# Performance work log

Hardware: AMD Instinct MI355X
Metric: run time of the kernel (lower is better)

The kernel has to match this reference:

```python
import jax, jax.numpy as jnp
import numpy as np

NX, NY = 256, 256            # img_size
NUM_DET, VIEW = 368, 180
SDD, SCD = 1000.0, 500.0
DCD = SDD - SCD
DET_INT = 2.0
PX = 1.0                     # pixel_size
SHIFT = 0.0                  # no quarter offset


def _geometry():
    # Faithful numpy port of FP.param_setting (equally_spaced mode)
    d_beta = np.pi * 360.0 / VIEW / 180.0
    beta = np.linspace(0.0, (VIEW - 1) * d_beta, VIEW)
    axis_x = np.linspace(-NX / 2, NX / 2, NX + 1) * PX          # [NX+1]
    axis_y = np.linspace(-NY / 2, NY / 2, NY + 1) * PX          # [NY+1]
    range_det_x = np.ones(NUM_DET) * DCD
    range_det_y = np.linspace(-(NUM_DET - 1) / 2, (NUM_DET - 1) / 2, NUM_DET) * DET_INT + SHIFT
    src = np.array([-SCD, 0.0])
    cb, sb = np.cos(beta), np.sin(beta)
    src_point = np.stack([src[0] * cb + src[1] * sb, -src[0] * sb + src[1] * cb])  # [2, V]
    det_x_rot = cb[None, :] * range_det_x[:, None] + sb[None, :] * range_det_y[:, None]   # [D, V]
    det_y_rot = -sb[None, :] * range_det_x[:, None] + cb[None, :] * range_det_y[:, None]  # [D, V]
    ax = (axis_x[:, None] - src_point[0][None, :])[None, :, :] / (det_x_rot - src_point[0])[:, None, :]  # [D, NX+1, V]
    ay = (axis_y[:, None] - src_point[1][None, :])[None, :, :] / (det_y_rot - src_point[1])[:, None, :]  # [D, NY+1, V]
    a_min = np.maximum(np.minimum(ax[:, 0, :], ax[:, -1, :]), np.minimum(ay[:, 0, :], ay[:, -1, :]))
    a_min[a_min < 0] = 0.0
    a_max = np.minimum(np.maximum(ax[:, 0, :], ax[:, -1, :]), np.maximum(ay[:, 0, :], ay[:, -1, :]))
    a_max[a_max > 1] = 1.0
    axy = np.concatenate([ax, ay], axis=1)                       # [D, NX+NY+2, V]
    axy[(axy > a_max[:, None, :]) | (axy < a_min[:, None, :])] = np.nan
    axy = np.sort(axy, axis=1)                                   # NaNs sort to the end (matches torch)
    diff_axy = np.diff(axy, n=1, axis=1)                         # [D, S, V], S = NX+NY+1
    a_mid = axy[:, :-1, :] + diff_axy / 2
    diff_axy = np.nan_to_num(diff_axy, nan=0.0)
    a_mid = np.nan_to_num(a_mid, nan=0.0)
    s2d = np.sqrt((det_x_rot - src_point[0]) ** 2 + (det_y_rot - src_point[1]) ** 2)  # [D, V]
    weighting = diff_axy.transpose(0, 2, 1)[None, None] * s2d[None, None, :, :, None]  # [1,1,D,V,S]
    x_pos = a_mid * (det_x_rot[:, None, :] - src_point[0]) + src_point[0]
    x_pos = x_pos.transpose(0, 2, 1) / (PX * (NX - 1) / 2)       # [D, V, S]
    y_pos = a_mid * (det_y_rot[:, None, :] - src_point[1]) + src_point[1]
    y_pos = y_pos.transpose(0, 2, 1) / (PX * (NY - 1) / 2)
    grid_pos = np.stack([x_pos, y_pos], axis=-1)                 # [D, V, S, 2]
    return grid_pos.astype(np.float32), weighting.astype(np.float32)


def _bilinear_sample(img, gx, gy):
    # torch.nn.functional.grid_sample: bilinear, padding_mode='zeros', align_corners=False
    # img: [B,C,H,W]; gx indexes W, gy indexes H; gx/gy: [D,V,S]
    B, C, H, W = img.shape
    ix = ((gx + 1.0) * W - 1.0) * 0.5
    iy = ((gy + 1.0) * H - 1.0) * 0.5
    ix0 = jnp.floor(ix)
    iy0 = jnp.floor(iy)
    wx1 = ix - ix0
    wy1 = iy - iy0
    out = jnp.zeros((B, C) + gx.shape, dtype=img.dtype)
    for dx in (0, 1):
        for dy in (0, 1):
            xi = ix0 + dx
            yi = iy0 + dy
            w = (wx1 if dx else 1.0 - wx1) * (wy1 if dy else 1.0 - wy1)
            valid = (xi >= 0) & (xi < W) & (yi >= 0) & (yi < H)
            xi_c = jnp.clip(xi, 0, W - 1).astype(jnp.int32)
            yi_c = jnp.clip(yi, 0, H - 1).astype(jnp.int32)
            out = out + img[:, :, yi_c, xi_c] * (w * valid)[None, None]
    return out  # [B,C,D,V,S]


def setup_inputs() -> dict:
    key = jax.random.key(0)
    img = jax.random.normal(key, (1, 1, NX, NY), dtype=jnp.float32)
    gp, wt = _geometry()
    return {"img": img, "grid_pos": jnp.asarray(gp), "weighting": jnp.asarray(wt)}


def reference(img, grid_pos, weighting):
    # All views vectorized at once (torch version loops over views)
    interp = _bilinear_sample(img, grid_pos[..., 0], grid_pos[..., 1])  # [B,C,D,V,S]
    sino = jnp.sum(weighting * interp, axis=-1)                         # [B,C,D,V]
    return jnp.where(jnp.isnan(sino), jnp.zeros((), sino.dtype), sino)
```

## Files before the change

kernel.cpp:

```cpp
#include <hip/hip_runtime.h>
#include <hip/hip_fp16.h>
#include <math.h>


constexpr int IMG_N  = 256;
constexpr int NDET   = 368;
constexpr int NVIEW  = 180;
constexpr int NSAMP  = 2 * IMG_N + 1;
constexpr int DV     = NDET * NVIEW;
constexpr int NITER  = (NSAMP + 63) / 64;

struct __align__(8) Corner { __half2 ab; __half2 cd; };

constexpr size_t PACK_BYTES = (size_t)IMG_N * IMG_N * sizeof(Corner);
constexpr size_t RT_OFF     = PACK_BYTES;
constexpr size_t RT_BYTES   = (size_t)DV * 3 * sizeof(float4);
constexpr size_t KR_OFF     = RT_OFF + RT_BYTES;
constexpr size_t KR_BYTES   = (size_t)DV * sizeof(int2);
constexpr size_t WS_NEEDED  = KR_OFF + KR_BYTES;

__device__ __forceinline__ double valAP(double A, double s, double inv, int k) {
    return (A + s * (double)k) * inv;
}

__global__ __launch_bounds__(256) void pack_kernel(
    const float* __restrict__ img, Corner* __restrict__ P)
{
    const int idx = blockIdx.x * 256 + threadIdx.x;
    const int y  = idx >> 8;
    const int x  = idx & 255;
    const int x1 = min(x + 1, IMG_N - 1);
    const int y1 = min(y + 1, IMG_N - 1);
    Corner c;
    c.ab = __floats2half2_rn(img[y * IMG_N + x],  img[y * IMG_N + x1]);
    c.cd = __floats2half2_rn(img[y1 * IMG_N + x], img[y1 * IMG_N + x1]);
    P[idx] = c;
}

__global__ __launch_bounds__(256) void geom_kernel(
    float4* __restrict__ rt, int2* __restrict__ kr)
{
    const int idx = blockIdx.x * 256 + threadIdx.x;
    if (idx >= DV) return;
    const int d = idx / NVIEW;
    const int v = idx - d * NVIEW;

    const double d_beta = ((M_PI * 360.0) / (double)NVIEW) / 180.0;
    const double stop   = (double)(NVIEW - 1) * d_beta;
    const double step   = stop / (double)(NVIEW - 1);
    const double beta   = (v == NVIEW - 1) ? stop : (double)v * step;
    const double cb = cos(beta), sb = sin(beta);

    const double sx  = -500.0 * cb;
    const double sy  =  500.0 * sb;
    const double rdy = ((double)d - 183.5) * 2.0;
    const double dx  = cb * 500.0 + sb * rdy;
    const double dy  = (-sb) * 500.0 + cb * rdy;
    const double ddx = dx - sx, ddy = dy - sy;

    double Ax, sxn;
    const double invx = 1.0 / ddx;
    if (invx >= 0.0) { Ax = -128.0 - sx; sxn = 1.0; }
    else             { Ax =  128.0 - sx; sxn = -1.0; }
    double Ay, syn;
    const double invy = 1.0 / ddy;
    if (invy >= 0.0) { Ay = -128.0 - sy; syn = 1.0; }
    else             { Ay =  128.0 - sy; syn = -1.0; }

    const double vx0 = valAP(Ax, sxn, invx, 0), vxN = valAP(Ax, sxn, invx, IMG_N);
    const double vy0 = valAP(Ay, syn, invy, 0), vyN = valAP(Ay, syn, invy, IMG_N);
    double a_min = fmax(vx0, vy0); if (a_min < 0.0) a_min = 0.0;
    double a_max = fmin(vxN, vyN); if (a_max > 1.0) a_max = 1.0;

    const double absdx = fabs(ddx), absdy = fabs(ddy);

    int klox, khix, kloy, khiy;
    {
        double kd = (a_min - vx0) * absdx;
        kd = fmin(fmax(kd, -1.0), 258.0);
        int k = (int)kd; k = max(0, min(k, 256));
        while (k > 0    && valAP(Ax, sxn, invx, k - 1) >= a_min) --k;
        while (k <= 256 && valAP(Ax, sxn, invx, k) < a_min)      ++k;
        klox = k;
        kd = (a_max - vx0) * absdx;
        kd = fmin(fmax(kd, -1.0), 258.0);
        k = (int)kd; k = max(0, min(k, 256));
        while (k > 0    && valAP(Ax, sxn, invx, k - 1) > a_max)  --k;
        while (k <= 256 && valAP(Ax, sxn, invx, k) <= a_max)     ++k;
        khix = k - 1;
        if (klox > khix) { klox = 0; khix = -1; }
    }
    {
        double kd = (a_min - vy0) * absdy;
        kd = fmin(fmax(kd, -1.0), 258.0);
        int k = (int)kd; k = max(0, min(k, 256));
        while (k > 0    && valAP(Ay, syn, invy, k - 1) >= a_min) --k;
        while (k <= 256 && valAP(Ay, syn, invy, k) < a_min)      ++k;
        kloy = k;
        kd = (a_max - vy0) * absdy;
        kd = fmin(fmax(kd, -1.0), 258.0);
        k = (int)kd; k = max(0, min(k, 256));
        while (k > 0    && valAP(Ay, syn, invy, k - 1) > a_max)  --k;
        while (k <= 256 && valAP(Ay, syn, invy, k) <= a_max)     ++k;
        khiy = k - 1;
        if (kloy > khiy) { kloy = 0; khiy = -1; }
    }

    const int nx = khix - klox + 1;
    const int ny = khiy - kloy + 1;
    const double s2d = sqrt(ddx * ddx + ddy * ddy);

    const double sxd = sxn * invx, syd = syn * invy;
    const double bxd = (Ax + sxn * (double)klox) * invx;
    const double byd = (Ay + syn * (double)kloy) * invy;
    const double ssum = sxd + syd;
    const double c0 = (byd - bxd) / ssum;
    const double c1 = syd / ssum;

    float4* o = rt + (size_t)idx * 3;
    o[0] = make_float4((float)bxd, (float)sxd, (float)byd, (float)syd);
    o[1] = make_float4((float)c0, (float)c1, (float)s2d, 0.0f);
    o[2] = make_float4((float)(ddx * (128.0 / 127.5)),
                       (float)(sx  * (128.0 / 127.5) + 127.5),
                       (float)(ddy * (128.0 / 127.5)),
                       (float)(sy  * (128.0 / 127.5) + 127.5));
    kr[idx] = make_int2(nx, ny);
}

__device__ __forceinline__ float mergedq(int q, float bx, float sx, float by,
                                         float sy, float c0, float c1,
                                         int nx, int ny)
{
    const int t   = q + 1;
    const int mlo = max(0, t - ny);
    const int mhi = min(nx, t);
    int m = (int)fmaf((float)q, c1, c0);
    m = max(mlo, min(m, mhi));
    while (m > mlo) {
        const int mm = m - 1;
        const bool Pmm = (t - 1 - mm < 0) || (mm >= nx) ||
            (fmaf((float)(t - 1 - mm), sy, by) <= fmaf((float)mm, sx, bx));
        if (!Pmm) break;
        m = mm;
    }
    while (m < mhi) {
        const bool Pm = (t - 1 - m < 0) || (m >= nx) ||
            (fmaf((float)(t - 1 - m), sy, by) <= fmaf((float)m, sx, bx));
        if (Pm) break;
        ++m;
    }
    const float xl = (m > 0)     ? fmaf((float)(m - 1),     sx, bx) : -3e38f;
    const float yl = (t - m > 0) ? fmaf((float)(t - 1 - m), sy, by) : -3e38f;
    return fmaxf(xl, yl);
}

__global__ __launch_bounds__(256) void fp_siddon(
    const Corner* __restrict__ P,
    const float4* __restrict__ rt,
    const int2*   __restrict__ kr,
    float*        __restrict__ out)
{
    const int wave = threadIdx.x >> 6;
    const int lane = threadIdx.x & 63;
    const int dv   = __builtin_amdgcn_readfirstlane(blockIdx.x * 4 + wave);

    const float4 A = rt[(size_t)dv * 3 + 0];
    const float4 B = rt[(size_t)dv * 3 + 1];
    const float4 C = rt[(size_t)dv * 3 + 2];
    const int2 nn = kr[dv];
    const int nx = nn.x, ny = nn.y;
    const int M = nx + ny;
    const int npairs = M - 1;

    float acc = 0.0f;

    for (int base = 0; base < npairs; base += 64) {
        const int p = base + lane;
        const bool act = (p < npairs);
        const int q = act ? p + 1 : 1;

        const float cur = mergedq(q, A.x, A.y, A.z, A.w, B.x, B.y, nx, ny);
        float prev = __shfl_up(cur, 1, 64);
        if (lane == 0)
            prev = mergedq(base, A.x, A.y, A.z, A.w, B.x, B.y, nx, ny);

        const float diff = cur - prev;
        const float mid  = fmaf(diff, 0.5f, prev);
        const float ixp  = fmaf(mid, C.x, C.y);
        const float iyp  = fmaf(mid, C.z, C.w);
        const float wf   = act ? diff * B.z : 0.0f;

        const float fx0 = floorf(ixp), fy0 = floorf(iyp);
        const float wx1 = ixp - fx0,  wy1 = iyp - fy0;
        const int x0 = (int)fx0, y0 = (int)fy0;
        const int xc = min(max(x0, 0), IMG_N - 1);
        const int yb = min(max(y0, 0), IMG_N - 1);

        const Corner pc = P[yb * IMG_N + xc];
        const float2 r0 = __half22float2(pc.ab);
        const float2 r1 = __half22float2(pc.cd);

        const bool loX = (x0 == -1), loY = (y0 == -1);
        const float a  = r0.x;
        const float b2 = loX ? r0.x : r0.y;
        const float d2 = loX ? r1.x : r1.y;
        const float c3 = loY ? a  : r1.x;
        const float d3 = loY ? b2 : d2;
        const float x0v = (((unsigned)x0)       < 256u) ? 1.0f : 0.0f;
        const float x1v = (((unsigned)(x0 + 1)) < 256u) ? 1.0f : 0.0f;
        const float my0 = (((unsigned)y0)       < 256u) ? 1.0f : 0.0f;
        const float my1 = (((unsigned)(y0 + 1)) < 256u) ? 1.0f : 0.0f;
        const float wx0 = 1.0f - wx1;
        const float wy0 = (1.0f - wy1) * my0;
        const float wy1m = wy1 * my1;
        const float interp = (a * x0v * wx0 + b2 * x1v * wx1) * wy0
                           + (c3 * x0v * wx0 + d3 * x1v * wx1) * wy1m;

        acc = fmaf(wf, interp, acc);
    }

    #pragma unroll
    for (int off = 32; off > 0; off >>= 1)
        acc += __shfl_down(acc, off, 64);
    if (lane == 0)
        out[dv] = isnan(acc) ? 0.0f : acc;
}

__global__ __launch_bounds__(256) void fp_kernel_nopack(
    const float*  __restrict__ img,
    const float2* __restrict__ grid,
    const float*  __restrict__ wt,
    float*        __restrict__ out)
{
    const int wave = threadIdx.x >> 6;
    const int lane = threadIdx.x & 63;
    const int dv   = blockIdx.x * 4 + wave;
    const long base = (long)dv * NSAMP;

    float2 g[NITER];
    float  w[NITER];
    #pragma unroll
    for (int k = 0; k < NITER; ++k) {
        const int s = lane + k * 64;
        if (s < NSAMP) { g[k] = grid[base + s]; w[k] = wt[base + s]; }
        else           { g[k] = make_float2(0.0f, 0.0f); w[k] = 0.0f; }
    }
    float acc = 0.0f;
    #pragma unroll
    for (int k = 0; k < NITER; ++k) {
        const float ix = ((g[k].x + 1.0f) * 256.0f - 1.0f) * 0.5f;
        const float iy = ((g[k].y + 1.0f) * 256.0f - 1.0f) * 0.5f;
        const float fx0 = floorf(ix), fy0 = floorf(iy);
        const float wx1 = ix - fx0,  wy1 = iy - fy0;
        const int x0 = (int)fx0, y0 = (int)fy0;
        const int xc  = min(max(x0, 0), IMG_N - 2);
        const int yc0 = min(max(y0, 0), IMG_N - 1);
        const int yc1 = min(max(y0 + 1, 0), IMG_N - 1);
        const float2 p0 = *(const float2*)(img + yc0 * IMG_N + xc);
        const float2 p1 = *(const float2*)(img + yc1 * IMG_N + xc);
        const bool x0v = ((unsigned)x0) < 256u;
        const bool x1v = ((unsigned)(x0 + 1)) < 256u;
        const bool hiX = (x0 == IMG_N - 1);
        const bool loX = (x0 == -1);
        const float v00 = x0v ? (hiX ? p0.y : p0.x) : 0.0f;
        const float v01 = x1v ? (loX ? p0.x : p0.y) : 0.0f;
        const float v10 = x0v ? (hiX ? p1.y : p1.x) : 0.0f;
        const float v11 = x1v ? (loX ? p1.x : p1.y) : 0.0f;
        const float my0 = (((unsigned)y0) < 256u) ? 1.0f : 0.0f;
        const float my1 = (((unsigned)(y0 + 1)) < 256u) ? 1.0f : 0.0f;
        const float wx0 = 1.0f - wx1;
        const float wy0 = (1.0f - wy1) * my0;
        const float wy1m = wy1 * my1;
        acc += w[k] * ((v00 * wx0 + v01 * wx1) * wy0
                     + (v10 * wx0 + v11 * wx1) * wy1m);
    }
    #pragma unroll
    for (int off = 32; off > 0; off >>= 1)
        acc += __shfl_down(acc, off, 64);
    if (lane == 0) out[dv] = isnan(acc) ? 0.0f : acc;
}

extern "C" void kernel_launch(void* const* d_in, const int* in_sizes, int n_in,
                              void* d_out, int out_size, void* d_ws, size_t ws_size,
                              hipStream_t stream) {
    const float*  img  = (const float*)d_in[0];
    const float2* grid = (const float2*)d_in[1];
    const float*  wt   = (const float*)d_in[2];
    float*        out  = (float*)d_out;

    if (ws_size >= WS_NEEDED) {
        Corner* P  = (Corner*)d_ws;
        float4* rt = (float4*)((char*)d_ws + RT_OFF);
        int2*   kr = (int2*)  ((char*)d_ws + KR_OFF);
        pack_kernel<<<IMG_N * IMG_N / 256, 256, 0, stream>>>(img, P);
        geom_kernel<<<(DV + 255) / 256, 256, 0, stream>>>(rt, kr);
        fp_siddon<<<DV / 4, 256, 0, stream>>>(P, rt, kr, out);
    } else {
        fp_kernel_nopack<<<DV / 4, 256, 0, stream>>>(img, grid, wt, out);
    }
}
```

Before: 412.7 us.

## Enumerate Siddon crossings per plane with local rank search and transposed corner table

Each lane now owns one crossing (an x-plane or a y-plane index) rather than one position in the merged sorted order. It finds the next crossing with a short local search against the other axis. This removes the merge-rank search over both sequences and the cross-lane shuffle plus the extra lane-0 recompute. A transposed packed corner table is added so lanes on y-plane crossings read a layout whose consecutive samples sit next to each other in memory. This doubles the packing work and the workspace, adds a divergent branch between the x and y paths, and changes tie handling between coincident crossings.

```diff
diff --git a/kernel.cpp b/kernel.cpp
--- a/kernel.cpp
+++ b/kernel.cpp
@@ -13,7 +13,8 @@
 struct __align__(8) Corner { __half2 ab; __half2 cd; };
 
 constexpr size_t PACK_BYTES = (size_t)IMG_N * IMG_N * sizeof(Corner);
-constexpr size_t RT_OFF     = PACK_BYTES;
+constexpr size_t PT_OFF     = PACK_BYTES;
+constexpr size_t RT_OFF     = 2 * PACK_BYTES;
 constexpr size_t RT_BYTES   = (size_t)DV * 3 * sizeof(float4);
 constexpr size_t KR_OFF     = RT_OFF + RT_BYTES;
 constexpr size_t KR_BYTES   = (size_t)DV * sizeof(int2);
@@ -24,17 +25,29 @@
 }
 
 __global__ __launch_bounds__(256) void pack_kernel(
-    const float* __restrict__ img, Corner* __restrict__ P)
+    const float* __restrict__ img, Corner* __restrict__ P, Corner* __restrict__ PT)
 {
     const int idx = blockIdx.x * 256 + threadIdx.x;
-    const int y  = idx >> 8;
-    const int x  = idx & 255;
-    const int x1 = min(x + 1, IMG_N - 1);
-    const int y1 = min(y + 1, IMG_N - 1);
-    Corner c;
-    c.ab = __floats2half2_rn(img[y * IMG_N + x],  img[y * IMG_N + x1]);
-    c.cd = __floats2half2_rn(img[y1 * IMG_N + x], img[y1 * IMG_N + x1]);
-    P[idx] = c;
+    if (idx < IMG_N * IMG_N) {
+        const int y  = idx >> 8;
+        const int x  = idx & 255;
+        const int x1 = min(x + 1, IMG_N - 1);
+        const int y1 = min(y + 1, IMG_N - 1);
+        Corner c;
+        c.ab = __floats2half2_rn(img[y * IMG_N + x],  img[y * IMG_N + x1]);
+        c.cd = __floats2half2_rn(img[y1 * IMG_N + x], img[y1 * IMG_N + x1]);
+        P[idx] = c;
+    } else {
+        const int k  = idx - IMG_N * IMG_N;
+        const int x  = k >> 8;
+        const int y  = k & 255;
+        const int x1 = min(x + 1, IMG_N - 1);
+        const int y1 = min(y + 1, IMG_N - 1);
+        Corner c;
+        c.ab = __floats2half2_rn(img[y * IMG_N + x],  img[y1 * IMG_N + x]);
+        c.cd = __floats2half2_rn(img[y * IMG_N + x1], img[y1 * IMG_N + x1]);
+        PT[k] = c;
+    }
 }
 
 __global__ __launch_bounds__(256) void geom_kernel(
@@ -113,13 +126,12 @@
     const double sxd = sxn * invx, syd = syn * invy;
     const double bxd = (Ax + sxn * (double)klox) * invx;
     const double byd = (Ay + syn * (double)kloy) * invy;
-    const double ssum = sxd + syd;
-    const double c0 = (byd - bxd) / ssum;
-    const double c1 = syd / ssum;
+    const double invsxd = 1.0 / sxd;
+    const double invsyd = 1.0 / syd;
 
     float4* o = rt + (size_t)idx * 3;
     o[0] = make_float4((float)bxd, (float)sxd, (float)byd, (float)syd);
-    o[1] = make_float4((float)c0, (float)c1, (float)s2d, 0.0f);
+    o[1] = make_float4((float)invsxd, (float)invsyd, (float)s2d, 0.0f);
     o[2] = make_float4((float)(ddx * (128.0 / 127.5)),
                        (float)(sx  * (128.0 / 127.5) + 127.5),
                        (float)(ddy * (128.0 / 127.5)),
@@ -127,35 +139,9 @@
     kr[idx] = make_int2(nx, ny);
 }
 
-__device__ __forceinline__ float mergedq(int q, float bx, float sx, float by,
-                                         float sy, float c0, float c1,
-                                         int nx, int ny)
-{
-    const int t   = q + 1;
-    const int mlo = max(0, t - ny);
-    const int mhi = min(nx, t);
-    int m = (int)fmaf((float)q, c1, c0);
-    m = max(mlo, min(m, mhi));
-    while (m > mlo) {
-        const int mm = m - 1;
-        const bool Pmm = (t - 1 - mm < 0) || (mm >= nx) ||
-            (fmaf((float)(t - 1 - mm), sy, by) <= fmaf((float)mm, sx, bx));
-        if (!Pmm) break;
-        m = mm;
-    }
-    while (m < mhi) {
-        const bool Pm = (t - 1 - m < 0) || (m >= nx) ||
-            (fmaf((float)(t - 1 - m), sy, by) <= fmaf((float)m, sx, bx));
-        if (Pm) break;
-        ++m;
-    }
-    const float xl = (m > 0)     ? fmaf((float)(m - 1),     sx, bx) : -3e38f;
-    const float yl = (t - m > 0) ? fmaf((float)(t - 1 - m), sy, by) : -3e38f;
-    return fmaxf(xl, yl);
-}
-
 __global__ __launch_bounds__(256) void fp_siddon(
     const Corner* __restrict__ P,
+    const Corner* __restrict__ PT,
     const float4* __restrict__ rt,
     const int2*   __restrict__ kr,
     float*        __restrict__ out)
@@ -170,35 +156,56 @@
     const int2 nn = kr[dv];
     const int nx = nn.x, ny = nn.y;
     const int M = nx + ny;
-    const int npairs = M - 1;
 
     float acc = 0.0f;
 
-    for (int base = 0; base < npairs; base += 64) {
-        const int p = base + lane;
-        const bool act = (p < npairs);
-        const int q = act ? p + 1 : 1;
-
-        const float cur = mergedq(q, A.x, A.y, A.z, A.w, B.x, B.y, nx, ny);
-        float prev = __shfl_up(cur, 1, 64);
-        if (lane == 0)
-            prev = mergedq(base, A.x, A.y, A.z, A.w, B.x, B.y, nx, ny);
-
-        const float diff = cur - prev;
-        const float mid  = fmaf(diff, 0.5f, prev);
+    for (int base = 0; base < M; base += 64) {
+        int c = base + lane;
+        const bool act = (c < M);
+        c = act ? c : (M - 1);
+        const bool isX = (c < nx);
+
+        float cur, nxt;
+        if (isX) {
+            cur = fmaf((float)c, A.y, A.x);
+            int j = (int)((cur - A.z) * B.y);
+            j = max(0, min(j, ny));
+            while (j > 0  && fmaf((float)(j - 1), A.w, A.z) >= cur) --j;
+            while (j < ny && fmaf((float)j,       A.w, A.z) <  cur) ++j;
+            nxt = 3.0e38f;
+            if (c + 1 < nx) nxt = fmaf((float)(c + 1), A.y, A.x);
+            if (j < ny)     nxt = fminf(nxt, fmaf((float)j, A.w, A.z));
+        } else {
+            const int cy = c - nx;
+            cur = fmaf((float)cy, A.w, A.z);
+            int i = (int)((cur - A.x) * B.x);
+            i = max(0, min(i, nx));
+            while (i > 0  && fmaf((float)(i - 1), A.y, A.x) >  cur) --i;
+            while (i < nx && fmaf((float)i,       A.y, A.x) <= cur) ++i;
+            nxt = 3.0e38f;
+            if (cy + 1 < ny) nxt = fmaf((float)(cy + 1), A.w, A.z);
+            if (i < nx)      nxt = fminf(nxt, fmaf((float)i, A.y, A.x));
+        }
+
+        const bool valid = act && (nxt < 2.9e38f);
+        if (!valid) nxt = cur;
+        const float diff = nxt - cur;
+        const float mid  = fmaf(diff, 0.5f, cur);
+        const float wf   = valid ? diff * B.z : 0.0f;
         const float ixp  = fmaf(mid, C.x, C.y);
         const float iyp  = fmaf(mid, C.z, C.w);
-        const float wf   = act ? diff * B.z : 0.0f;
 
         const float fx0 = floorf(ixp), fy0 = floorf(iyp);
         const float wx1 = ixp - fx0,  wy1 = iyp - fy0;
         const int x0 = (int)fx0, y0 = (int)fy0;
         const int xc = min(max(x0, 0), IMG_N - 1);
-        const int yb = min(max(y0, 0), IMG_N - 1);
-
-        const Corner pc = P[yb * IMG_N + xc];
-        const float2 r0 = __half22float2(pc.ab);
-        const float2 r1 = __half22float2(pc.cd);
+        const int yc = min(max(y0, 0), IMG_N - 1);
+
+        const Corner pc = isX ? P[(yc << 8) + xc] : PT[(xc << 8) + yc];
+        const float2 u  = __half22float2(pc.ab);
+        const float2 w2 = __half22float2(pc.cd);
+        const float2 r0 = isX ? u  : make_float2(u.x, w2.x);
+        const float2 r1 = isX ? w2 : make_float2(u.y, w2.y);
 
         const bool loX = (x0 == -1), loY = (y0 == -1);
         const float a  = r0.x;
@@ -290,11 +297,12 @@
 
     if (ws_size >= WS_NEEDED) {
         Corner* P  = (Corner*)d_ws;
+        Corner* PT = (Corner*)((char*)d_ws + PT_OFF);
         float4* rt = (float4*)((char*)d_ws + RT_OFF);
         int2*   kr = (int2*)  ((char*)d_ws + KR_OFF);
-        pack_kernel<<<IMG_N * IMG_N / 256, 256, 0, stream>>>(img, P);
+        pack_kernel<<<2 * IMG_N * IMG_N / 256, 256, 0, stream>>>(img, P, PT);
         geom_kernel<<<(DV + 255) / 256, 256, 0, stream>>>(rt, kr);
-        fp_siddon<<<DV / 4, 256, 0, stream>>>(P, rt, kr, out);
+        fp_siddon<<<DV / 4, 256, 0, stream>>>(P, PT, rt, kr, out);
     } else {
         fp_kernel_nopack<<<DV / 4, 256, 0, stream>>>(img, grid, wt, out);
     }
```

New measurement: 445.7 us. 8.0% more time.
